# Kernel optimization log

Measured on AMD Instinct MI355X. Metric: run time of the kernel, lower is better.

The kernel has to match this reference:

```python
import jax, jax.numpy as jnp
import numpy as np

N_NODES = 50000
N_EDGES = 800000
D_IN = 128
D_OUT = 128


def setup_inputs() -> dict:
    key = jax.random.key(0)
    k1, k2, k3, k4 = jax.random.split(key, 4)
    node_features = jax.random.normal(k1, (N_NODES, D_IN), dtype=jnp.float32)
    edge_index = jax.random.randint(k2, (2, N_EDGES), 0, N_NODES, dtype=jnp.int64)
    # nn.Linear params: weight [out, in], bias [out]
    W = jax.random.normal(k3, (D_OUT, D_IN), dtype=jnp.float32) / np.sqrt(D_IN)
    b = jax.random.normal(k4, (D_OUT,), dtype=jnp.float32) * 0.01
    return {"node_features": node_features, "edge_index": edge_index, "W": W, "b": b}


def reference(node_features, edge_index, W, b):
    source_nodes = edge_index[0]
    dest_nodes = edge_index[1]
    # gather neighbor features [E, D_in], scatter-add into [N, D_in]
    neighbor_features = node_features[source_nodes]
    aggregated = jax.ops.segment_sum(neighbor_features, dest_nodes,
                                     num_segments=node_features.shape[0])
    # nn.Linear: x @ W.T + b
    return aggregated @ W.T + b
```

## Files before the change

### kernel.cpp

```cpp
#include <hip/hip_runtime.h>


constexpr int NN = 50000;
constexpr int NE = 800000;
constexpr int D  = 128;

constexpr int BS  = 256;
constexpr int NB  = (NN + BS - 1) / BS;
constexpr int CAP = 8192;
constexpr int EPB = 4096;
constexpr int NBLK_B = (NE + EPB - 1) / EPB;

typedef __attribute__((ext_vector_type(8))) short bf16x8;
typedef __attribute__((ext_vector_type(4))) float f32x4;

__device__ inline unsigned short f2bf(float f) {
    unsigned u = __float_as_uint(f);
    return (unsigned short)((u + 0x7fffu + ((u >> 16) & 1u)) >> 16);
}
__device__ inline float bflo(unsigned v) { return __uint_as_float(v << 16); }
__device__ inline float bfhi(unsigned v) { return __uint_as_float(v & 0xffff0000u); }

constexpr int NF4 = NN * D / 4;
constexpr int W4  = D * D / 4;
constexpr int NBLK_P = (NF4 + W4 + 255) / 256;
constexpr int GRID_A = NBLK_B + NBLK_P;

__global__ __launch_bounds__(256) void k_prep_bucket(
    const float* __restrict__ nf, const float* __restrict__ W,
    const int* __restrict__ ei,
    ushort* __restrict__ nfh, ushort* __restrict__ Wh,
    int* __restrict__ cursor, unsigned* __restrict__ buf)
{
    __shared__ int h[NB];
    __shared__ int gbase[NB];
    __shared__ int lcur[NB];
    const int t = threadIdx.x;

    if (blockIdx.x < NBLK_B) {
        for (int i = t; i < NB; i += 256) { h[i] = 0; lcur[i] = 0; }
        __syncthreads();
        const int e0 = blockIdx.x * EPB;
        unsigned pk[16];
        #pragma unroll
        for (int j = 0; j < 16; ++j) {
            int e = e0 + j * 256 + t;
            if (e < NE) {
                unsigned s = (unsigned)ei[e];
                unsigned d = (unsigned)ei[NE + e];
                pk[j] = (d << 16) | s;
                atomicAdd(&h[pk[j] >> 24], 1);
            }
        }
        __syncthreads();
        for (int i = t; i < NB; i += 256)
            if (h[i] > 0) gbase[i] = i * CAP + atomicAdd(&cursor[i], h[i]);
        __syncthreads();
        #pragma unroll
        for (int j = 0; j < 16; ++j) {
            int e = e0 + j * 256 + t;
            if (e < NE) {
                unsigned b = pk[j] >> 24;
                int l = atomicAdd(&lcur[b], 1);
                buf[gbase[b] + l] = pk[j];
            }
        }
    } else {
        int i = (blockIdx.x - NBLK_B) * 256 + t;
        if (i < NF4) {
            float4 v = ((const float4*)nf)[i];
            ((ushort4*)nfh)[i] = make_ushort4(f2bf(v.x), f2bf(v.y), f2bf(v.z), f2bf(v.w));
        } else if (i < NF4 + W4) {
            int k = i - NF4;
            float4 v = ((const float4*)W)[k];
            ((ushort4*)Wh)[k] = make_ushort4(f2bf(v.x), f2bf(v.y), f2bf(v.z), f2bf(v.w));
        }
    }
}

__global__ __launch_bounds__(256) void k_sortlocal(const int* __restrict__ cursor,
                                                   const unsigned* __restrict__ buf,
                                                   ushort* __restrict__ srt,
                                                   int* __restrict__ beg,
                                                   int* __restrict__ end) {
    __shared__ int s[BS];
    __shared__ int cur[BS];
    const int b = blockIdx.x;
    const int t = threadIdx.x;
    const int seg = b * CAP;
    const int cnt = cursor[b];

    s[t] = 0; __syncthreads();
    for (int e = t; e < cnt; e += 256)
        atomicAdd(&s[(buf[seg + e] >> 16) & 255u], 1);
    __syncthreads();
    int myc = s[t];
    for (int off = 1; off < 256; off <<= 1) {
        int v = (t >= off) ? s[t - off] : 0;
        __syncthreads();
        s[t] += v;
        __syncthreads();
    }
    int excl = s[t] - myc;
    cur[t] = excl;
    int node = b * BS + t;
    if (node < NN) { beg[node] = seg + excl; end[node] = seg + excl + myc; }
    __syncthreads();

    for (int e = t; e < cnt; e += 256) {
        unsigned pk = buf[seg + e];
        int n = (pk >> 16) & 255u;
        int p = atomicAdd(&cur[n], 1);
        srt[seg + p] = (ushort)(pk & 0xffffu);
    }
}

constexpr int ROWU = 136;

__global__ __launch_bounds__(256) void k_agg_linear(
    const unsigned* __restrict__ nfh, const ushort* __restrict__ srt,
    const int* __restrict__ beg, const int* __restrict__ end,
    const ushort* __restrict__ Wh, const float* __restrict__ bias,
    float* __restrict__ out)
{
    __shared__ unsigned tile[16 * ROWU / 2];
    const int t = threadIdx.x, lane = t & 63, w = t >> 6;
    const int base = blockIdx.x * 16;

    #pragma unroll
    for (int i = 0; i < 4; ++i) {
        const int node = base + w * 4 + i;
        int p = beg[node];
        const int e = end[node];
        float ax=0.f, ay=0.f, bx=0.f, by=0.f, cx=0.f, cy=0.f, dx=0.f, dy=0.f;
        for (; p + 7 < e; p += 8) {
            int e0 = srt[p+0]; int e1 = srt[p+1];
            int e2 = srt[p+2]; int e3 = srt[p+3];
            int e4 = srt[p+4]; int e5 = srt[p+5];
            int e6 = srt[p+6]; int e7 = srt[p+7];
            unsigned v0 = nfh[(size_t)e0 * 64 + lane];
            unsigned v1 = nfh[(size_t)e1 * 64 + lane];
            unsigned v2 = nfh[(size_t)e2 * 64 + lane];
            unsigned v3 = nfh[(size_t)e3 * 64 + lane];
            unsigned v4 = nfh[(size_t)e4 * 64 + lane];
            unsigned v5 = nfh[(size_t)e5 * 64 + lane];
            unsigned v6 = nfh[(size_t)e6 * 64 + lane];
            unsigned v7 = nfh[(size_t)e7 * 64 + lane];
            ax += bflo(v0); ay += bfhi(v0);
            bx += bflo(v1); by += bfhi(v1);
            cx += bflo(v2); cy += bfhi(v2);
            dx += bflo(v3); dy += bfhi(v3);
            ax += bflo(v4); ay += bfhi(v4);
            bx += bflo(v5); by += bfhi(v5);
            cx += bflo(v6); cy += bfhi(v6);
            dx += bflo(v7); dy += bfhi(v7);
        }
        for (; p < e; ++p) {
            unsigned v0 = nfh[(size_t)srt[p] * 64 + lane];
            ax += bflo(v0); ay += bfhi(v0);
        }
        float rx = (ax + bx) + (cx + dx);
        float ry = (ay + by) + (cy + dy);
        tile[(w * 4 + i) * (ROWU / 2) + lane] =
            (unsigned)f2bf(rx) | ((unsigned)f2bf(ry) << 16);
    }
    __syncthreads();

    const int m = lane & 15, q = lane >> 4;
    const ushort* lds = (const ushort*)tile;
    bf16x8 a[4];
    #pragma unroll
    for (int kk = 0; kk < 4; ++kk)
        a[kk] = *(const bf16x8*)(lds + m * ROWU + q * 8 + kk * 32);

    #pragma unroll
    for (int cc = 0; cc < 2; ++cc) {
        const int c0 = w * 32 + cc * 16;
        float bv = bias[c0 + m];
        f32x4 acc = { bv, bv, bv, bv };
        const ushort* wrow = Wh + (size_t)(c0 + m) * D + q * 8;
        #pragma unroll
        for (int kk = 0; kk < 4; ++kk) {
            bf16x8 bb = *(const bf16x8*)(wrow + kk * 32);
            acc = __builtin_amdgcn_mfma_f32_16x16x32_bf16(a[kk], bb, acc, 0, 0, 0);
        }
        float* op = out + (size_t)(base + q * 4) * D + c0 + m;
        op[0]     = acc[0];
        op[D]     = acc[1];
        op[2 * D] = acc[2];
        op[3 * D] = acc[3];
    }
}

extern "C" void kernel_launch(void* const* d_in, const int* in_sizes, int n_in,
                              void* d_out, int out_size, void* d_ws, size_t ws_size,
                              hipStream_t stream) {
    const float* nf = (const float*)d_in[0];
    const int*   ei = (const int*)d_in[1];
    const float* W  = (const float*)d_in[2];
    const float* b  = (const float*)d_in[3];
    float* out = (float*)d_out;

    ushort*   nfh  = (ushort*)d_ws;
    ushort*   Wh   = nfh + (size_t)NN * D;
    unsigned* buf  = (unsigned*)(Wh + D * D);
    ushort*   srt  = (ushort*)(buf + NB * CAP);
    int*      cursor = (int*)(srt + NB * CAP);
    int*      beg  = cursor + NB;
    int*      end  = beg + NN;

    hipMemsetAsync(cursor, 0, NB * sizeof(int), stream);
    k_prep_bucket<<<GRID_A, 256, 0, stream>>>(nf, W, ei, nfh, Wh, cursor, buf);
    k_sortlocal  <<<NB, 256, 0, stream>>>(cursor, buf, srt, beg, end);
    k_agg_linear <<<NN / 16, 256, 0, stream>>>((const unsigned*)nfh, srt, beg, end, Wh, b, out);
}
```

Measured before the change: 156.4 us.

## Use one wavefront per node in aggregation and smaller dest buckets

The aggregation kernel now uses 1024-thread blocks with one wavefront per destination node instead of four nodes per wavefront, so there is more parallelism in flight to hide gather latency. The edge loop is branch-free with masked, clamped loads in groups of eight. Destination buckets shrink from 256 to 128 nodes, with smaller capacity, and the local sort runs with 512 threads. The cost is more buckets and blocks, masked wasted loads on low-degree nodes, half the waves idle during the MFMA phase, and a higher overflow risk from the smaller per-bucket capacity.

```diff
diff --git a/kernel.cpp b/kernel.cpp
--- a/kernel.cpp
+++ b/kernel.cpp
@@ -5,9 +5,9 @@
 constexpr int NE = 800000;
 constexpr int D  = 128;
 
-constexpr int BS  = 256;
+constexpr int BS  = 128;
 constexpr int NB  = (NN + BS - 1) / BS;
-constexpr int CAP = 8192;
+constexpr int CAP = 4096;
 constexpr int EPB = 4096;
 constexpr int NBLK_B = (NE + EPB - 1) / EPB;
 
@@ -49,7 +49,7 @@
                 unsigned s = (unsigned)ei[e];
                 unsigned d = (unsigned)ei[NE + e];
                 pk[j] = (d << 16) | s;
-                atomicAdd(&h[pk[j] >> 24], 1);
+                atomicAdd(&h[pk[j] >> 23], 1);
             }
         }
         __syncthreads();
@@ -60,7 +60,7 @@
         for (int j = 0; j < 16; ++j) {
             int e = e0 + j * 256 + t;
             if (e < NE) {
-                unsigned b = pk[j] >> 24;
+                unsigned b = pk[j] >> 23;
                 int l = atomicAdd(&lcur[b], 1);
                 buf[gbase[b] + l] = pk[j];
             }
@@ -78,7 +78,7 @@
     }
 }
 
-__global__ __launch_bounds__(256) void k_sortlocal(const int* __restrict__ cursor,
+__global__ __launch_bounds__(512) void k_sortlocal(const int* __restrict__ cursor,
                                                    const unsigned* __restrict__ buf,
                                                    ushort* __restrict__ srt,
                                                    int* __restrict__ beg,
@@ -90,26 +90,29 @@
     const int seg = b * CAP;
     const int cnt = cursor[b];
 
-    s[t] = 0; __syncthreads();
-    for (int e = t; e < cnt; e += 256)
-        atomicAdd(&s[(buf[seg + e] >> 16) & 255u], 1);
-    __syncthreads();
-    int myc = s[t];
-    for (int off = 1; off < 256; off <<= 1) {
-        int v = (t >= off) ? s[t - off] : 0;
-        __syncthreads();
-        s[t] += v;
-        __syncthreads();
-    }
-    int excl = s[t] - myc;
-    cur[t] = excl;
-    int node = b * BS + t;
-    if (node < NN) { beg[node] = seg + excl; end[node] = seg + excl + myc; }
-    __syncthreads();
-
-    for (int e = t; e < cnt; e += 256) {
+    if (t < BS) s[t] = 0;
+    __syncthreads();
+    for (int e = t; e < cnt; e += 512)
+        atomicAdd(&s[(buf[seg + e] >> 16) & (BS - 1)], 1);
+    __syncthreads();
+    int myc = (t < BS) ? s[t] : 0;
+    for (int off = 1; off < BS; off <<= 1) {
+        int v = (t >= off && t < BS) ? s[t - off] : 0;
+        __syncthreads();
+        if (t < BS) s[t] += v;
+        __syncthreads();
+    }
+    if (t < BS) {
+        int excl = s[t] - myc;
+        cur[t] = excl;
+        int node = b * BS + t;
+        if (node < NN) { beg[node] = seg + excl; end[node] = seg + excl + myc; }
+    }
+    __syncthreads();
+
+    for (int e = t; e < cnt; e += 512) {
         unsigned pk = buf[seg + e];
-        int n = (pk >> 16) & 255u;
+        int n = (pk >> 16) & (BS - 1);
         int p = atomicAdd(&cur[n], 1);
         srt[seg + p] = (ushort)(pk & 0xffffu);
     }
@@ -117,7 +120,7 @@
 
 constexpr int ROWU = 136;
 
-__global__ __launch_bounds__(256) void k_agg_linear(
+__global__ __launch_bounds__(1024) void k_agg_linear(
     const unsigned* __restrict__ nfh, const ushort* __restrict__ srt,
     const int* __restrict__ beg, const int* __restrict__ end,
     const ushort* __restrict__ Wh, const float* __restrict__ bias,
@@ -126,56 +129,44 @@
     __shared__ unsigned tile[16 * ROWU / 2];
     const int t = threadIdx.x, lane = t & 63, w = t >> 6;
     const int base = blockIdx.x * 16;
-
-    #pragma unroll
-    for (int i = 0; i < 4; ++i) {
-        const int node = base + w * 4 + i;
-        int p = beg[node];
-        const int e = end[node];
-        float ax=0.f, ay=0.f, bx=0.f, by=0.f, cx=0.f, cy=0.f, dx=0.f, dy=0.f;
-        for (; p + 7 < e; p += 8) {
-            int e0 = srt[p+0]; int e1 = srt[p+1];
-            int e2 = srt[p+2]; int e3 = srt[p+3];
-            int e4 = srt[p+4]; int e5 = srt[p+5];
-            int e6 = srt[p+6]; int e7 = srt[p+7];
-            unsigned v0 = nfh[(size_t)e0 * 64 + lane];
-            unsigned v1 = nfh[(size_t)e1 * 64 + lane];
-            unsigned v2 = nfh[(size_t)e2 * 64 + lane];
-            unsigned v3 = nfh[(size_t)e3 * 64 + lane];
-            unsigned v4 = nfh[(size_t)e4 * 64 + lane];
-            unsigned v5 = nfh[(size_t)e5 * 64 + lane];
-            unsigned v6 = nfh[(size_t)e6 * 64 + lane];
-            unsigned v7 = nfh[(size_t)e7 * 64 + lane];
-            ax += bflo(v0); ay += bfhi(v0);
-            bx += bflo(v1); by += bfhi(v1);
-            cx += bflo(v2); cy += bfhi(v2);
-            dx += bflo(v3); dy += bfhi(v3);
-            ax += bflo(v4); ay += bfhi(v4);
-            bx += bflo(v5); by += bfhi(v5);
-            cx += bflo(v6); cy += bfhi(v6);
-            dx += bflo(v7); dy += bfhi(v7);
-        }
-        for (; p < e; ++p) {
-            unsigned v0 = nfh[(size_t)srt[p] * 64 + lane];
-            ax += bflo(v0); ay += bfhi(v0);
-        }
-        float rx = (ax + bx) + (cx + dx);
-        float ry = (ay + by) + (cy + dy);
-        tile[(w * 4 + i) * (ROWU / 2) + lane] =
-            (unsigned)f2bf(rx) | ((unsigned)f2bf(ry) << 16);
-    }
-    __syncthreads();
-
-    const int m = lane & 15, q = lane >> 4;
-    const ushort* lds = (const ushort*)tile;
-    bf16x8 a[4];
-    #pragma unroll
-    for (int kk = 0; kk < 4; ++kk)
-        a[kk] = *(const bf16x8*)(lds + m * ROWU + q * 8 + kk * 32);
-
-    #pragma unroll
-    for (int cc = 0; cc < 2; ++cc) {
-        const int c0 = w * 32 + cc * 16;
+    const int node = base + w;
+
+    int p = beg[node];
+    const int e = end[node];
+    float ax=0.f, ay=0.f, bx=0.f, by=0.f, cx=0.f, cy=0.f, dx=0.f, dy=0.f;
+    for (; p < e; p += 8) {
+        const int lim = e - 1;
+        unsigned v[8]; float msk[8];
+        #pragma unroll
+        for (int j = 0; j < 8; ++j) {
+            int pos = p + j;
+            msk[j] = (pos <= lim) ? 1.f : 0.f;
+            if (pos > lim) pos = lim;
+            v[j] = nfh[(size_t)srt[pos] * 64 + lane];
+        }
+        ax += msk[0] * bflo(v[0]); ay += msk[0] * bfhi(v[0]);
+        bx += msk[1] * bflo(v[1]); by += msk[1] * bfhi(v[1]);
+        cx += msk[2] * bflo(v[2]); cy += msk[2] * bfhi(v[2]);
+        dx += msk[3] * bflo(v[3]); dy += msk[3] * bfhi(v[3]);
+        ax += msk[4] * bflo(v[4]); ay += msk[4] * bfhi(v[4]);
+        bx += msk[5] * bflo(v[5]); by += msk[5] * bfhi(v[5]);
+        cx += msk[6] * bflo(v[6]); cy += msk[6] * bfhi(v[6]);
+        dx += msk[7] * bflo(v[7]); dy += msk[7] * bfhi(v[7]);
+    }
+    float rx = (ax + bx) + (cx + dx);
+    float ry = (ay + by) + (cy + dy);
+    tile[w * (ROWU / 2) + lane] = (unsigned)f2bf(rx) | ((unsigned)f2bf(ry) << 16);
+    __syncthreads();
+
+    if (w < 8) {
+        const int m = lane & 15, q = lane >> 4;
+        const ushort* lds = (const ushort*)tile;
+        bf16x8 a[4];
+        #pragma unroll
+        for (int kk = 0; kk < 4; ++kk)
+            a[kk] = *(const bf16x8*)(lds + m * ROWU + q * 8 + kk * 32);
+
+        const int c0 = w * 16;
         float bv = bias[c0 + m];
         f32x4 acc = { bv, bv, bv, bv };
         const ushort* wrow = Wh + (size_t)(c0 + m) * D + q * 8;
@@ -211,6 +202,6 @@
 
     hipMemsetAsync(cursor, 0, NB * sizeof(int), stream);
     k_prep_bucket<<<GRID_A, 256, 0, stream>>>(nf, W, ei, nfh, Wh, cursor, buf);
-    k_sortlocal  <<<NB, 256, 0, stream>>>(cursor, buf, srt, beg, end);
-    k_agg_linear <<<NN / 16, 256, 0, stream>>>((const unsigned*)nfh, srt, beg, end, Wh, b, out);
-}
+    k_sortlocal  <<<NB, 512, 0, stream>>>(cursor, buf, srt, beg, end);
+    k_agg_linear <<<NN / 16, 1024, 0, stream>>>((const unsigned*)nfh, srt, beg, end, Wh, b, out);
+}
```

Measured after the change: 145.6 us. -6.9%, faster.
